# Optimization experiments

Hardware: AMD Instinct MI355X
Metric: run time of the kernel (lower is better)

Reference implementation:

```python
import jax, jax.numpy as jnp
import numpy as np

D_MODEL = 1024
STATE_DIM = 64
SEQ_L = 2048


def hippo_legs_A(N):
    n = jnp.arange(N, dtype=jnp.float32)
    two_n1 = 2.0 * n + 1.0
    sq = jnp.sqrt(two_n1[:, None] * two_n1[None, :])
    A = jnp.tril(sq, k=-1) * -1.0
    return A + jnp.diag(-(n + 1.0))


def setup_inputs() -> dict:
    key = jax.random.key(0)
    kB, kC = jax.random.split(key)
    N = STATE_DIM
    n = jnp.arange(N, dtype=jnp.float32)
    B_ref = jnp.sqrt(2.0 * n + 1.0)  # (N,)
    B = jnp.tile(B_ref[None, :], (D_MODEL, 1)) + 0.01 * jax.random.normal(kB, (D_MODEL, N), dtype=jnp.float32)
    C = 0.1 * jax.random.normal(kC, (D_MODEL, N), dtype=jnp.float32)
    D = jnp.zeros((D_MODEL,), dtype=jnp.float32)
    log_dt = jnp.log(jnp.asarray(0.1, dtype=jnp.float32))
    return {"B": B, "C": C, "D": D, "log_dt": log_dt, "L": SEQ_L}


def reference(B, C, D, log_dt, L):
    N = B.shape[1]
    A = hippo_legs_A(N)                       # (N,N) continuous-time HiPPO-LegS
    dt = jax.nn.softplus(log_dt) + 1e-06
    I = jnp.eye(N, dtype=A.dtype)
    lhs = I - 0.5 * dt * A
    rhs = I + 0.5 * dt * A
    A_bar = jnp.linalg.solve(lhs, rhs)        # (N,N) bilinear discretization
    B_bar = jnp.linalg.solve(lhs, (dt * B).T).T  # (d_model, N)
    A_bar_T = A_bar.T

    def step(x, _):
        y = jnp.sum(C * x, axis=-1)           # (d_model,)
        return x @ A_bar_T, y

    _, ys = jax.lax.scan(step, B_bar, None, length=L)  # ys: (L, d_model)
    K = ys.T                                   # (d_model, L)
    K = K.at[:, 0].add(D)
    return K[:, None, :]                       # (d_model, 1, L)
```

## Files before the change

kernel.cpp:

```cpp
#include <hip/hip_runtime.h>

namespace {

template<int CTRL, int RM>
__device__ __forceinline__ float dpp_mov0(float v) {
  return __int_as_float(__builtin_amdgcn_update_dpp(
      0, __float_as_int(v), CTRL, RM, 0xF, false));
}
template<int CTRL, int RM>
__device__ __forceinline__ float dpp_mov1(float v) {
  return __int_as_float(__builtin_amdgcn_update_dpp(
      0x3f800000, __float_as_int(v), CTRL, RM, 0xF, false));
}

__device__ __forceinline__ float rl(float v, int k) {
  return __int_as_float(__builtin_amdgcn_readlane(__float_as_int(v), k));
}

struct Hoist {
  float cs0, cs1, cs2, cs3, cs4, cs5;
  float gs0, gs1, gs2, gs3, gs4, gs5;
  float r, inv_d, hr, alpha, k2;
};

__device__ __forceinline__ Hoist make_hoist(float dt, int n) {
  float h = 0.5f * dt, fn = (float)n;
  float r = sqrtf(2.f * fn + 1.f);
  float d = 1.f + h * (fn + 1.f);
  float inv_d = 1.f / d;
  float g = (1.f - h * fn) * inv_d;
  float c = g - 1.f;
  Hoist H;
  H.r = r; H.inv_d = inv_d; H.hr = h * r;
  H.alpha = 1.f + h * fn;
  H.k2 = r * (2.f - d) * inv_d;
#define COEF_STEP(IDX, CTRL, RM)                                        \
  H.cs##IDX = c; H.gs##IDX = g;                                         \
  { float cP = dpp_mov0<CTRL, RM>(c);                                   \
    float gP = dpp_mov1<CTRL, RM>(g);                                   \
    c = fmaf(g, cP, c); g = g * gP; }
  COEF_STEP(0, 0x111, 0xF)
  COEF_STEP(1, 0x112, 0xF)
  COEF_STEP(2, 0x114, 0xF)
  COEF_STEP(3, 0x118, 0xF)
  COEF_STEP(4, 0x142, 0xA)
  COEF_STEP(5, 0x143, 0xC)
#undef COEF_STEP
  return H;
}

__device__ __forceinline__ float abar_apply(float x, const Hoist& H) {
  float w1 = H.r * x, w2 = H.k2 * x;
#define APPLY_STEP(IDX, CTRL, RM)                                       \
  { float w1P = dpp_mov0<CTRL, RM>(w1);                                 \
    float w2P = dpp_mov0<CTRL, RM>(w2);                                 \
    w2 = fmaf(H.cs##IDX, w1P, fmaf(H.gs##IDX, w2P, w2));                \
    w1 += w1P; }
  APPLY_STEP(0, 0x111, 0xF)
  APPLY_STEP(1, 0x112, 0xF)
  APPLY_STEP(2, 0x114, 0xF)
  APPLY_STEP(3, 0x118, 0xF)
  APPLY_STEP(4, 0x142, 0xA)
  APPLY_STEP(5, 0x143, 0xC)
#undef APPLY_STEP
  float tp = dpp_mov0<0x138, 0xF>(w2);
  return H.inv_d * fmaf(-H.hr, w1 + tp, H.alpha * x);
}

template<int CTRL, int RM>
__device__ __forceinline__ void linrec_step(float& G, float& W) {
  float Wo = dpp_mov0<CTRL, RM>(W);
  float Go = dpp_mov1<CTRL, RM>(G);
  W = fmaf(G, Wo, W);
  G *= Go;
}
__device__ __forceinline__ float lhs_solve(float z, const Hoist& H) {
  float G = H.gs0, W = H.r * z * H.inv_d;
  linrec_step<0x111, 0xF>(G, W);
  linrec_step<0x112, 0xF>(G, W);
  linrec_step<0x114, 0xF>(G, W);
  linrec_step<0x118, 0xF>(G, W);
  linrec_step<0x142, 0xA>(G, W);
  linrec_step<0x143, 0xC>(G, W);
  float sp = dpp_mov0<0x138, 0xF>(W);
  return (z - H.hr * sp) * H.inv_d;
}

__device__ __forceinline__ float softplus_dt(float ldt) {
  return log1pf(expf(ldt)) + 1e-6f;
}

__device__ __forceinline__ float grow_matvec(const float* __restrict__ M,
                                             float u, int lane) {
  float a0 = 0.f, a1 = 0.f, a2 = 0.f, a3 = 0.f;
  const float4* m4 = (const float4*)(M + lane * 64);
  #pragma unroll
  for (int q = 0; q < 16; ++q) {
    float4 f = m4[q];
    a0 = fmaf(f.x, rl(u, 4 * q + 0), a0);
    a1 = fmaf(f.y, rl(u, 4 * q + 1), a1);
    a2 = fmaf(f.z, rl(u, 4 * q + 2), a2);
    a3 = fmaf(f.w, rl(u, 4 * q + 3), a3);
  }
  return (a0 + a1) + (a2 + a3);
}

__device__ __forceinline__ float q2t_matvec(const float* Q2T, float u, int lane) {
  float a0 = 0.f, a1 = 0.f, a2 = 0.f, a3 = 0.f;
  #pragma unroll
  for (int k = 0; k < 64; k += 4) {
    float q0 = Q2T[(k + 0) * 64 + lane];
    float q1 = Q2T[(k + 1) * 64 + lane];
    float q2 = Q2T[(k + 2) * 64 + lane];
    float q3 = Q2T[(k + 3) * 64 + lane];
    a0 = fmaf(q0, rl(u, k + 0), a0);
    a1 = fmaf(q1, rl(u, k + 1), a1);
    a2 = fmaf(q2, rl(u, k + 2), a2);
    a3 = fmaf(q3, rl(u, k + 3), a3);
  }
  return (a0 + a1) + (a2 + a3);
}

}

__global__ __launch_bounds__(64) void hippo_pow(const float* __restrict__ ldt_p,
                                                float* __restrict__ A32c,
                                                float* __restrict__ QROW,
                                                float* __restrict__ Q2ROW) {
  const int lane = threadIdx.x;
  const int m = blockIdx.x;
  const float dt = softplus_dt(ldt_p[0]);
  const Hoist H = make_hoist(dt, lane);
  float x = (lane == m) ? 1.f : 0.f;
  #pragma unroll 1
  for (int s = 0; s < 32; ++s) x = abar_apply(x, H);
  A32c[lane * 64 + m] = x;
  #pragma unroll 1
  for (int s = 0; s < 32; ++s) x = abar_apply(x, H);
  QROW[m * 64 + lane] = x;
  #pragma unroll 1
  for (int s = 0; s < 64; ++s) x = abar_apply(x, H);
  Q2ROW[m * 64 + lane] = x;
}

__global__ __launch_bounds__(256, 4) void hippo_main(
    const float* __restrict__ B, const float* __restrict__ C,
    const float* __restrict__ Dv, const float* __restrict__ ldt_p,
    const float* __restrict__ A32c, const float* __restrict__ QROW,
    const float* __restrict__ Q2ROW, float* __restrict__ out, int NI, int L) {
  __shared__ __align__(16) float Vl[64 * 64];
  __shared__ __align__(16) float Ul[32 * 64];
  __shared__ __align__(16) float Q2T[64 * 64];
  const int d = blockIdx.x;
  const int tau = threadIdx.x;
  const int lane = tau & 63;
  const int w = tau >> 6;

  if (w == 0) {
    const Hoist H = make_hoist(softplus_dt(ldt_p[0]), lane);
    float v = lhs_solve(softplus_dt(ldt_p[0]) * B[d * 64 + lane], H);
    #pragma unroll 1
    for (int j = 0; j < 32; ++j) {
      Vl[j * 64 + (lane ^ (j & 31))] = v;
      if (j < 31) v = abar_apply(v, H);
    }
  } else if (w == 3) {
    const Hoist H = make_hoist(softplus_dt(ldt_p[0]), lane);
    float bb = lhs_solve(softplus_dt(ldt_p[0]) * B[d * 64 + lane], H);
    float v = grow_matvec(A32c, bb, lane);
    #pragma unroll 1
    for (int j = 32; j < 64; ++j) {
      Vl[j * 64 + (lane ^ (j & 31))] = v;
      if (j < 63) v = abar_apply(v, H);
    }
  } else {
    #pragma unroll
    for (int q = 0; q < 16; ++q) {
      float4 f = *(const float4*)(Q2ROW + lane * 64 + 4 * q);
      Q2T[(4 * q + 0) * 64 + lane] = f.x;
      Q2T[(4 * q + 1) * 64 + lane] = f.y;
      Q2T[(4 * q + 2) * 64 + lane] = f.z;
      Q2T[(4 * q + 3) * 64 + lane] = f.w;
    }
    if (w == 1) {
      float u = C[d * 64 + lane];
      const int nE = (NI + 1) >> 1;
      #pragma unroll 1
      for (int a = 0; a < nE; ++a) {
        Ul[(2 * a) * 64 + lane] = u;
        if (a < nE - 1) u = q2t_matvec(Q2T, u, lane);
      }
    } else {
      float u = grow_matvec(QROW, C[d * 64 + lane], lane);
      const int nO = NI >> 1;
      #pragma unroll 1
      for (int a = 0; a < nO; ++a) {
        Ul[(2 * a + 1) * 64 + lane] = u;
        if (a < nO - 1) u = q2t_matvec(Q2T, u, lane);
      }
    }
  }
  __syncthreads();

  const int j = lane;
  float acc[8];
  #pragma unroll
  for (int k = 0; k < 8; ++k) acc[k] = 0.f;
  #pragma unroll
  for (int h = 0; h < 4; ++h) {
    float vr[16];
    #pragma unroll
    for (int e = 0; e < 16; ++e)
      vr[e] = Vl[j * 64 + ((16 * h + e) ^ (j & 31))];
    #pragma unroll
    for (int k = 0; k < 8; ++k) {
      const int i = w + 4 * k;
      if (i < NI) {
        const float4* u4 = (const float4*)(Ul + i * 64 + 16 * h);
        float4 f0 = u4[0], f1 = u4[1], f2 = u4[2], f3 = u4[3];
        acc[k] = fmaf(vr[0],  f0.x, acc[k]);
        acc[k] = fmaf(vr[1],  f0.y, acc[k]);
        acc[k] = fmaf(vr[2],  f0.z, acc[k]);
        acc[k] = fmaf(vr[3],  f0.w, acc[k]);
        acc[k] = fmaf(vr[4],  f1.x, acc[k]);
        acc[k] = fmaf(vr[5],  f1.y, acc[k]);
        acc[k] = fmaf(vr[6],  f1.z, acc[k]);
        acc[k] = fmaf(vr[7],  f1.w, acc[k]);
        acc[k] = fmaf(vr[8],  f2.x, acc[k]);
        acc[k] = fmaf(vr[9],  f2.y, acc[k]);
        acc[k] = fmaf(vr[10], f2.z, acc[k]);
        acc[k] = fmaf(vr[11], f2.w, acc[k]);
        acc[k] = fmaf(vr[12], f3.x, acc[k]);
        acc[k] = fmaf(vr[13], f3.y, acc[k]);
        acc[k] = fmaf(vr[14], f3.z, acc[k]);
        acc[k] = fmaf(vr[15], f3.w, acc[k]);
      }
    }
  }
  #pragma unroll
  for (int k = 0; k < 8; ++k) {
    const int i = w + 4 * k;
    if (i < NI) {
      float y = acc[k];
      if ((i | j) == 0) y += Dv[d];
      out[(size_t)d * L + i * 64 + j] = y;
    }
  }
}

extern "C" void kernel_launch(void* const* d_in, const int* in_sizes, int n_in,
                              void* d_out, int out_size, void* d_ws, size_t ws_size,
                              hipStream_t stream) {
  const float* B   = (const float*)d_in[0];
  const float* C   = (const float*)d_in[1];
  const float* Dv  = (const float*)d_in[2];
  const float* ldt = (const float*)d_in[3];
  const int d_model = in_sizes[2];
  const int L = out_size / d_model;
  const int NI = L / 64;
  float* A32c  = (float*)d_ws;
  float* QROW  = (float*)d_ws + 4096;
  float* Q2ROW = (float*)d_ws + 8192;
  hippo_pow<<<64, 64, 0, stream>>>(ldt, A32c, QROW, Q2ROW);
  hippo_main<<<d_model, 256, 0, stream>>>(B, C, Dv, ldt, A32c, QROW, Q2ROW,
                                          (float*)d_out, NI, L);
}
```

Baseline: 45.57 us.

## Hold the Q row in registers and compute the U chain in one wave

```diff
diff --git a/kernel.cpp b/kernel.cpp
--- a/kernel.cpp
+++ b/kernel.cpp
@@ -90,6 +90,28 @@
   return log1pf(expf(ldt)) + 1e-6f;
 }
 
+__device__ __forceinline__ void load_row_g(const float* __restrict__ base,
+                                           float (&pc)[64]) {
+  const float4* p4 = (const float4*)base;
+  #pragma unroll
+  for (int q = 0; q < 16; ++q) {
+    float4 f = p4[q];
+    pc[4*q+0] = f.x; pc[4*q+1] = f.y; pc[4*q+2] = f.z; pc[4*q+3] = f.w;
+  }
+}
+
+__device__ __forceinline__ float qapply(const float (&pc)[64], float u) {
+  float a0 = 0.f, a1 = 0.f, a2 = 0.f, a3 = 0.f;
+  #pragma unroll
+  for (int k = 0; k < 64; k += 4) {
+    a0 = fmaf(pc[k + 0], rl(u, k + 0), a0);
+    a1 = fmaf(pc[k + 1], rl(u, k + 1), a1);
+    a2 = fmaf(pc[k + 2], rl(u, k + 2), a2);
+    a3 = fmaf(pc[k + 3], rl(u, k + 3), a3);
+  }
+  return (a0 + a1) + (a2 + a3);
+}
+
 __device__ __forceinline__ float grow_matvec(const float* __restrict__ M,
                                              float u, int lane) {
   float a0 = 0.f, a1 = 0.f, a2 = 0.f, a3 = 0.f;
@@ -105,28 +127,15 @@
   return (a0 + a1) + (a2 + a3);
 }
 
-__device__ __forceinline__ float q2t_matvec(const float* Q2T, float u, int lane) {
-  float a0 = 0.f, a1 = 0.f, a2 = 0.f, a3 = 0.f;
-  #pragma unroll
-  for (int k = 0; k < 64; k += 4) {
-    float q0 = Q2T[(k + 0) * 64 + lane];
-    float q1 = Q2T[(k + 1) * 64 + lane];
-    float q2 = Q2T[(k + 2) * 64 + lane];
-    float q3 = Q2T[(k + 3) * 64 + lane];
-    a0 = fmaf(q0, rl(u, k + 0), a0);
-    a1 = fmaf(q1, rl(u, k + 1), a1);
-    a2 = fmaf(q2, rl(u, k + 2), a2);
-    a3 = fmaf(q3, rl(u, k + 3), a3);
-  }
-  return (a0 + a1) + (a2 + a3);
+__device__ __forceinline__ int vidx(int j, int n) {
+  return j * 64 + ((((n >> 2) ^ (j & 15)) << 2) | (n & 3));
 }
 
 }
 
 __global__ __launch_bounds__(64) void hippo_pow(const float* __restrict__ ldt_p,
                                                 float* __restrict__ A32c,
-                                                float* __restrict__ QROW,
-                                                float* __restrict__ Q2ROW) {
+                                                float* __restrict__ QROW) {
   const int lane = threadIdx.x;
   const int m = blockIdx.x;
   const float dt = softplus_dt(ldt_p[0]);
@@ -138,71 +147,58 @@
   #pragma unroll 1
   for (int s = 0; s < 32; ++s) x = abar_apply(x, H);
   QROW[m * 64 + lane] = x;
-  #pragma unroll 1
-  for (int s = 0; s < 64; ++s) x = abar_apply(x, H);
-  Q2ROW[m * 64 + lane] = x;
-}
-
-__global__ __launch_bounds__(256, 4) void hippo_main(
+}
+
+__global__ __launch_bounds__(256, 2) void hippo_main(
     const float* __restrict__ B, const float* __restrict__ C,
     const float* __restrict__ Dv, const float* __restrict__ ldt_p,
     const float* __restrict__ A32c, const float* __restrict__ QROW,
-    const float* __restrict__ Q2ROW, float* __restrict__ out, int NI, int L) {
+    float* __restrict__ out, int NI, int L) {
   __shared__ __align__(16) float Vl[64 * 64];
   __shared__ __align__(16) float Ul[32 * 64];
-  __shared__ __align__(16) float Q2T[64 * 64];
   const int d = blockIdx.x;
   const int tau = threadIdx.x;
   const int lane = tau & 63;
   const int w = tau >> 6;
-
-  if (w == 0) {
-    const Hoist H = make_hoist(softplus_dt(ldt_p[0]), lane);
-    float v = lhs_solve(softplus_dt(ldt_p[0]) * B[d * 64 + lane], H);
+  const int role = (w + d) & 3;
+  const float dt = softplus_dt(ldt_p[0]);
+
+  if (role == 0) {
+    const Hoist H = make_hoist(dt, lane);
+    float v = lhs_solve(dt * B[d * 64 + lane], H);
     #pragma unroll 1
     for (int j = 0; j < 32; ++j) {
-      Vl[j * 64 + (lane ^ (j & 31))] = v;
+      Vl[vidx(j, lane)] = v;
       if (j < 31) v = abar_apply(v, H);
     }
-  } else if (w == 3) {
-    const Hoist H = make_hoist(softplus_dt(ldt_p[0]), lane);
-    float bb = lhs_solve(softplus_dt(ldt_p[0]) * B[d * 64 + lane], H);
+  } else if (role == 3) {
+    const Hoist H = make_hoist(dt, lane);
+    float bb = lhs_solve(dt * B[d * 64 + lane], H);
     float v = grow_matvec(A32c, bb, lane);
     #pragma unroll 1
     for (int j = 32; j < 64; ++j) {
-      Vl[j * 64 + (lane ^ (j & 31))] = v;
+      Vl[vidx(j, lane)] = v;
       if (j < 63) v = abar_apply(v, H);
     }
-  } else {
-    #pragma unroll
-    for (int q = 0; q < 16; ++q) {
-      float4 f = *(const float4*)(Q2ROW + lane * 64 + 4 * q);
-      Q2T[(4 * q + 0) * 64 + lane] = f.x;
-      Q2T[(4 * q + 1) * 64 + lane] = f.y;
-      Q2T[(4 * q + 2) * 64 + lane] = f.z;
-      Q2T[(4 * q + 3) * 64 + lane] = f.w;
-    }
-    if (w == 1) {
-      float u = C[d * 64 + lane];
-      const int nE = (NI + 1) >> 1;
-      #pragma unroll 1
-      for (int a = 0; a < nE; ++a) {
-        Ul[(2 * a) * 64 + lane] = u;
-        if (a < nE - 1) u = q2t_matvec(Q2T, u, lane);
-      }
-    } else {
-      float u = grow_matvec(QROW, C[d * 64 + lane], lane);
-      const int nO = NI >> 1;
-      #pragma unroll 1
-      for (int a = 0; a < nO; ++a) {
-        Ul[(2 * a + 1) * 64 + lane] = u;
-        if (a < nO - 1) u = q2t_matvec(Q2T, u, lane);
-      }
+  } else if (role == 1) {
+    float pc[64];
+    load_row_g(QROW + lane * 64, pc);
+    float u = C[d * 64 + lane];
+    #pragma unroll 1
+    for (int i = 0; i < NI; ++i) {
+      Ul[i * 64 + lane] = u;
+      if (i < NI - 1) u = qapply(pc, u);
     }
   }
   __syncthreads();
 
   const int j = lane;
+  float ureg[8];
+  #pragma unroll
+  for (int k = 0; k < 8; ++k) {
+    const int i = w + 4 * k;
+    ureg[k] = (i < NI) ? Ul[i * 64 + lane] : 0.f;
+  }
   float acc[8];
   #pragma unroll
   for (int k = 0; k < 8; ++k) acc[k] = 0.f;
@@ -210,30 +206,16 @@
   for (int h = 0; h < 4; ++h) {
     float vr[16];
     #pragma unroll
-    for (int e = 0; e < 16; ++e)
-      vr[e] = Vl[j * 64 + ((16 * h + e) ^ (j & 31))];
+    for (int q4 = 0; q4 < 4; ++q4) {
+      const int q = h * 4 + q4;
+      float4 f = *(const float4*)&Vl[j * 64 + ((q ^ (j & 15)) << 2)];
+      vr[4*q4+0] = f.x; vr[4*q4+1] = f.y; vr[4*q4+2] = f.z; vr[4*q4+3] = f.w;
+    }
     #pragma unroll
     for (int k = 0; k < 8; ++k) {
-      const int i = w + 4 * k;
-      if (i < NI) {
-        const float4* u4 = (const float4*)(Ul + i * 64 + 16 * h);
-        float4 f0 = u4[0], f1 = u4[1], f2 = u4[2], f3 = u4[3];
-        acc[k] = fmaf(vr[0],  f0.x, acc[k]);
-        acc[k] = fmaf(vr[1],  f0.y, acc[k]);
-        acc[k] = fmaf(vr[2],  f0.z, acc[k]);
-        acc[k] = fmaf(vr[3],  f0.w, acc[k]);
-        acc[k] = fmaf(vr[4],  f1.x, acc[k]);
-        acc[k] = fmaf(vr[5],  f1.y, acc[k]);
-        acc[k] = fmaf(vr[6],  f1.z, acc[k]);
-        acc[k] = fmaf(vr[7],  f1.w, acc[k]);
-        acc[k] = fmaf(vr[8],  f2.x, acc[k]);
-        acc[k] = fmaf(vr[9],  f2.y, acc[k]);
-        acc[k] = fmaf(vr[10], f2.z, acc[k]);
-        acc[k] = fmaf(vr[11], f2.w, acc[k]);
-        acc[k] = fmaf(vr[12], f3.x, acc[k]);
-        acc[k] = fmaf(vr[13], f3.y, acc[k]);
-        acc[k] = fmaf(vr[14], f3.z, acc[k]);
-        acc[k] = fmaf(vr[15], f3.w, acc[k]);
+      #pragma unroll
+      for (int e = 0; e < 16; ++e) {
+        acc[k] = fmaf(vr[e], rl(ureg[k], 16 * h + e), acc[k]);
       }
     }
   }
@@ -258,10 +240,9 @@
   const int d_model = in_sizes[2];
   const int L = out_size / d_model;
   const int NI = L / 64;
-  float* A32c  = (float*)d_ws;
-  float* QROW  = (float*)d_ws + 4096;
-  float* Q2ROW = (float*)d_ws + 8192;
-  hippo_pow<<<64, 64, 0, stream>>>(ldt, A32c, QROW, Q2ROW);
-  hippo_main<<<d_model, 256, 0, stream>>>(B, C, Dv, ldt, A32c, QROW, Q2ROW,
-                                          (float*)d_out, NI, L);
-}
+  float* A32c = (float*)d_ws;
+  float* QROW = (float*)d_ws + 4096;
+  hippo_pow<<<64, 64, 0, stream>>>(ldt, A32c, QROW);
+  hippo_main<<<1024, 256, 0, stream>>>(B, C, Dv, ldt, A32c, QROW,
+                                       (float*)d_out, NI, L);
+}
```

Result: faster. 43.68 us (-4.2%).
